# Kernel optimization log

Hardware: AMD Instinct MI355X
Metric: run time of the kernel (lower is better)

Reference implementation:

```python
import jax, jax.numpy as jnp
import numpy as np

HEADS = 8
DIM_HEAD = 64

def setup_inputs() -> dict:
    key = jax.random.key(0)
    ks = jax.random.split(key, 9)
    B, N1, N2, D = 4, 2048, 2048, 1024
    inner = HEADS * DIM_HEAD  # 512
    s_in = 1.0 / np.sqrt(D)
    s_inner = 1.0 / np.sqrt(inner)
    return {
        "x1": jax.random.normal(ks[0], (B, N1, D), jnp.float32),
        "x2": jax.random.normal(ks[1], (B, N2, D), jnp.float32),
        "Wq1": jax.random.normal(ks[2], (D, inner), jnp.float32) * s_in,
        "Wk1": jax.random.normal(ks[3], (D, inner), jnp.float32) * s_in,
        "Wv1": jax.random.normal(ks[4], (D, inner), jnp.float32) * s_in,
        "Wk2": jax.random.normal(ks[5], (D, inner), jnp.float32) * s_in,
        "Wv2": jax.random.normal(ks[6], (D, inner), jnp.float32) * s_in,
        "Wo": jax.random.normal(ks[7], (inner, D), jnp.float32) * s_inner,
        "bo": jnp.zeros((D,), jnp.float32),
    }

def reference(x1, x2, Wq1, Wk1, Wv1, Wk2, Wv2, Wo, bo):
    h, d = HEADS, DIM_HEAD
    scale = d ** (-0.5)
    B, N1, _ = x1.shape
    N2 = x2.shape[1]

    def split_heads(t, n):
        return t.reshape(B, n, h, d)  # [B, n, h, d]

    q1 = split_heads(x1 @ Wq1, N1)
    k1 = split_heads(x1 @ Wk1, N1)
    v1 = split_heads(x1 @ Wv1, N1)
    k2 = split_heads(x2 @ Wk2, N2)
    v2 = split_heads(x2 @ Wv2, N2)

    k = jnp.concatenate([k1, k2], axis=1)  # [B, N1+N2, h, d]
    v = jnp.concatenate([v1, v2], axis=1)

    # fp32 precision for QK^T (matches _ATTN_PRECISION == 'fp32')
    sim = jnp.einsum('bihd,bjhd->bhij', q1.astype(jnp.float32),
                     k.astype(jnp.float32)) * scale  # [B, h, N1, N1+N2]
    attn = jax.nn.softmax(sim, axis=-1)
    out = jnp.einsum('bhij,bjhd->bihd', attn, v)  # [B, N1, h, d]
    out = out.reshape(B, N1, h * d)
    return out @ Wo + bo
```

## Files before the change

### kernel.cpp

```cpp
#include <hip/hip_runtime.h>
#include <stdint.h>

typedef __bf16 bf16x8 __attribute__((ext_vector_type(8)));
typedef float f32x4 __attribute__((ext_vector_type(4)));
typedef unsigned short ushort_t;

#define MFMA16(a,b,c) __builtin_amdgcn_mfma_f32_16x16x32_bf16((a),(b),(c),0,0,0)

__device__ __forceinline__ unsigned short f2bf(float f){
    unsigned u = __builtin_bit_cast(unsigned, f);
    u += 0x7fffu + ((u>>16)&1u);
    return (unsigned short)(u>>16);
}
__device__ __forceinline__ unsigned pack2bf(float lo, float hi){
    unsigned a = __builtin_bit_cast(unsigned, lo) + 0x8000u;
    unsigned b = __builtin_bit_cast(unsigned, hi) + 0x8000u;
    return __builtin_amdgcn_perm(b, a, 0x07060302u);
}
__device__ __forceinline__ float fexp2(float x){
#if __has_builtin(__builtin_amdgcn_exp2f)
    return __builtin_amdgcn_exp2f(x);
#else
    return exp2f(x);
#endif
}

__device__ __forceinline__ void async16(ushort_t* lds, const ushort_t* g){
#if __has_builtin(__builtin_amdgcn_global_load_lds)
    __builtin_amdgcn_global_load_lds(
        (const __attribute__((address_space(1))) void*)g,
        (__attribute__((address_space(3))) void*)lds, 16, 0, 0);
#else
    const int l = (int)(threadIdx.x & 63u);
    *(uint4*)(lds + (size_t)l*8) = *(const uint4*)g;
#endif
}

__global__ __launch_bounds__(256) void convert_x(const float* __restrict__ src,
                                                 ushort_t* __restrict__ dst){
    size_t i = ((size_t)blockIdx.x*256 + threadIdx.x)*8;
    float4 a = *(const float4*)(src + i);
    float4 b = *(const float4*)(src + i + 4);
    uint4 o;
    o.x = pack2bf(a.x, a.y); o.y = pack2bf(a.z, a.w);
    o.z = pack2bf(b.x, b.y); o.w = pack2bf(b.z, b.w);
    *(uint4*)(dst + i) = o;
}

__global__ __launch_bounds__(256) void transpose_w(
    const float* __restrict__ w0, const float* __restrict__ w1,
    const float* __restrict__ w2, const float* __restrict__ w3,
    const float* __restrict__ w4,
    ushort_t* __restrict__ Wt1, ushort_t* __restrict__ Wt2)
{
    int z = blockIdx.z;
    const float* src; ushort_t* dst;
    if (z < 3)  { src = (z==0)?w0:((z==1)?w1:w2); dst = Wt1 + (size_t)z*512*1024; }
    else        { src = (z==3)?w3:w4;             dst = Wt2 + (size_t)(z-3)*512*1024; }
    const int K = 1024, N = 512;
    int k0 = blockIdx.x*32, n0 = blockIdx.y*32;
    __shared__ float T[32][33];
    int t = threadIdx.x;
    int kr = t>>3, nc = (t&7)*4;
    float4 v = *(const float4*)(src + (size_t)(k0+kr)*N + n0 + nc);
    T[kr][nc] = v.x; T[kr][nc+1] = v.y; T[kr][nc+2] = v.z; T[kr][nc+3] = v.w;
    __syncthreads();
    int nr = t>>3, kc = (t&7)*4;
    uint2 o;
    o.x = pack2bf(T[kc][nr],   T[kc+1][nr]);
    o.y = pack2bf(T[kc+2][nr], T[kc+3][nr]);
    *(uint2*)(dst + (size_t)(n0+nr)*K + k0 + kc) = o;
    (void)K;
}

__global__ __launch_bounds__(256) void transpose_wo(
    const float* __restrict__ src, ushort_t* __restrict__ dst)
{
    __shared__ float T[64][33];
    const int k0 = blockIdx.x*64;
    const int n0 = blockIdx.y*32;
    const int t = threadIdx.x;
    const int kr = t>>3, nc = (t&7)*4;
#pragma unroll
    for (int hf = 0; hf < 2; ++hf){
        float4 v = *(const float4*)(src + (size_t)(k0 + hf*32 + kr)*1024 + n0 + nc);
        T[hf*32+kr][nc]   = v.x; T[hf*32+kr][nc+1] = v.y;
        T[hf*32+kr][nc+2] = v.z; T[hf*32+kr][nc+3] = v.w;
    }
    __syncthreads();
    const int nr = t>>3, kc = (t&7)*8;
    ushort_t tmp[8];
#pragma unroll
    for (int e = 0; e < 8; ++e){
        int dp = kc + e;
        int d  = ((dp&3)<<4) | (dp>>2);
        tmp[e] = f2bf(T[d][nr]);
    }
    *(uint4*)(dst + (size_t)(n0+nr)*512 + k0 + kc) = *(uint4*)tmp;
}

template<int KD, int MODE>
__global__ __launch_bounds__(256) void gemm_bt(
    const ushort_t* __restrict__ A, const ushort_t* __restrict__ Bt,
    ushort_t* __restrict__ Qp, ushort_t* __restrict__ Kp, ushort_t* __restrict__ Vtp,
    float* __restrict__ outF, const float* __restrict__ bias, int koff)
{
    __shared__ ushort_t As[2][128][32];
    __shared__ ushort_t Bs[2][128][32];
    const int t = threadIdx.x;
    const int m0 = blockIdx.x*128, n0 = blockIdx.y*128;
    const int w = t>>6, l = t&63;
    const int quad = l>>4, lc = l&15;
    const int wr = (w>>1)*64, wc = (w&1)*64;

    f32x4 acc[4][4] = {};

    const int crow = l>>2;
    const int kseg = (l&3)*8;
    const ushort_t* gA0 = A  + (size_t)(m0 + w*32      + crow)*KD + kseg;
    const ushort_t* gA1 = A  + (size_t)(m0 + w*32 + 16 + crow)*KD + kseg;
    const ushort_t* gB0 = Bt + (size_t)(n0 + w*32      + crow)*KD + kseg;
    const ushort_t* gB1 = Bt + (size_t)(n0 + w*32 + 16 + crow)*KD + kseg;

    const int NK = KD/32;

    async16(&As[0][w*32][0],    gA0);
    async16(&As[0][w*32+16][0], gA1);
    async16(&Bs[0][w*32][0],    gB0);
    async16(&Bs[0][w*32+16][0], gB1);
    __syncthreads();

    for (int kk = 0; kk < NK; ++kk) {
        const int cur = kk & 1;
        if (kk + 1 < NK) {
            const int k0 = (kk+1)*32;
            const int nx = cur ^ 1;
            async16(&As[nx][w*32][0],    gA0 + k0);
            async16(&As[nx][w*32+16][0], gA1 + k0);
            async16(&Bs[nx][w*32][0],    gB0 + k0);
            async16(&Bs[nx][w*32+16][0], gB1 + k0);
        }
        bf16x8 af[4], bfv[4];
#pragma unroll
        for (int i = 0; i < 4; ++i) {
            af[i]  = *(const bf16x8*)&As[cur][wr + i*16 + lc][quad*8];
            bfv[i] = *(const bf16x8*)&Bs[cur][wc + i*16 + lc][quad*8];
        }
#pragma unroll
        for (int mt = 0; mt < 4; ++mt)
#pragma unroll
            for (int nt = 0; nt < 4; ++nt)
                acc[mt][nt] = MFMA16(af[mt], bfv[nt], acc[mt][nt]);
        __syncthreads();
    }

    if (MODE == 2) {
        float bv[4];
#pragma unroll
        for (int nt = 0; nt < 4; ++nt) bv[nt] = bias[n0 + wc + nt*16 + lc];
#pragma unroll
        for (int mt = 0; mt < 4; ++mt) {
            const int row = m0 + wr + mt*16 + quad*4;
#pragma unroll
            for (int nt = 0; nt < 4; ++nt) {
                const int col = n0 + wc + nt*16 + lc;
#pragma unroll
                for (int r = 0; r < 4; ++r)
                    outF[(size_t)(row+r)*1024 + col] = acc[mt][nt][r] + bv[nt];
            }
        }
    } else {
        const int sub = (MODE == 0) ? (n0>>9) : (1 + (n0>>9));
        const int hh  = ((n0 + wc)>>6) & 7;
        const int dp  = 4*lc;
        const float QSC = 0.18033688011112042f;
        if (sub == 0) {
#pragma unroll
            for (int mt = 0; mt < 4; ++mt) {
                const int row = m0 + wr + mt*16 + quad*4;
                const int b = row>>11, i = row & 2047;
#pragma unroll
                for (int r = 0; r < 4; ++r) {
                    uint2 o;
                    o.x = pack2bf(acc[mt][0][r]*QSC, acc[mt][1][r]*QSC);
                    o.y = pack2bf(acc[mt][2][r]*QSC, acc[mt][3][r]*QSC);
                    *(uint2*)(Qp + ((size_t)(b*8+hh)*2048 + i + r)*64 + dp) = o;
                }
            }
        } else if (sub == 1) {
#pragma unroll
            for (int mt = 0; mt < 4; ++mt) {
                const int row = m0 + wr + mt*16 + quad*4;
                const int b = row>>11, i = row & 2047;
#pragma unroll
                for (int r = 0; r < 4; ++r) {
                    uint2 o;
                    o.x = pack2bf(acc[mt][0][r], acc[mt][1][r]);
                    o.y = pack2bf(acc[mt][2][r], acc[mt][3][r]);
                    *(uint2*)(Kp + ((size_t)(b*8+hh)*4096 + koff + i + r)*64 + dp) = o;
                }
            }
        } else {
#pragma unroll
            for (int mt = 0; mt < 4; ++mt) {
                const int row = m0 + wr + mt*16 + quad*4;
                const int b = row>>11, i = row & 2047;
#pragma unroll
                for (int nt = 0; nt < 4; ++nt) {
                    uint2 o;
                    o.x = pack2bf(acc[mt][nt][0], acc[mt][nt][1]);
                    o.y = pack2bf(acc[mt][nt][2], acc[mt][nt][3]);
                    *(uint2*)(Vtp + ((size_t)(b*8+hh)*64 + dp + nt)*4096 + koff + i) = o;
                }
            }
        }
    }
}

template<int SPLIT>
__global__ __launch_bounds__(256) void flash_attn_k(
    const ushort_t* __restrict__ Q, const ushort_t* __restrict__ Kg,
    const ushort_t* __restrict__ Vt, ushort_t* __restrict__ AO,
    float* __restrict__ P0, float* __restrict__ P1, float* __restrict__ Lp)
{
    constexpr int NJT = 64 / SPLIT;
    __shared__ ushort_t Ks[2][64][72];
    __shared__ ushort_t Vs[2][64][72];
    const int bh = blockIdx.x, qt = blockIdx.y;
    const int sp = (SPLIT > 1) ? (int)blockIdx.z : 0;
    const int jt0 = sp * NJT;
    const int b = bh>>3, h = bh&7;
    const int t = threadIdx.x, wv = t>>6, l = t&63;
    const int quad = l>>4, lc = l&15;

    const ushort_t* qbase = Q + ((size_t)bh*2048 + qt*128 + wv*16 + lc)*64;
    bf16x8 qA0 = *(const bf16x8*)(qbase + quad*8);
    bf16x8 qA1 = *(const bf16x8*)(qbase + 32 + quad*8);
    bf16x8 qB0 = *(const bf16x8*)(qbase + 64*64 + quad*8);
    bf16x8 qB1 = *(const bf16x8*)(qbase + 64*64 + 32 + quad*8);

    const ushort_t* Kb = Kg + (size_t)bh*4096*64;
    const ushort_t* Vb = Vt + (size_t)bh*64*4096;

    const int srow   = t>>2;
    const int schunk = t&3;
    const ushort_t* kst = Kb + (size_t)srow*64   + schunk*16;
    const ushort_t* vst = Vb + (size_t)srow*4096 + schunk*16;
    const int vcol = (schunk>>1)*32 + (schunk&1)*4;

    float l0 = 0.0f, l1 = 0.0f;
    f32x4 o0[4] = {}, o1[4] = {};

    const size_t kq0 = (size_t)jt0*64;
    uint4 ka  = *(const uint4*)(kst + kq0*64);
    uint4 kb2 = *(const uint4*)(kst + kq0*64 + 8);
    uint4 va  = *(const uint4*)(vst + kq0);
    uint4 vb2 = *(const uint4*)(vst + kq0 + 8);

    for (int jt = 0; jt < NJT; ++jt) {
        const int cur = jt & 1;
        ushort_t* ksd = &Ks[cur][srow][schunk*16];
        ushort_t* vsd = &Vs[cur][srow][vcol];
        *(uint4*)ksd     = ka;
        *(uint4*)(ksd+8) = kb2;
        { uint2 t0; t0.x = va.x;  t0.y = va.y;  *(uint2*)(vsd)      = t0; }
        { uint2 t1; t1.x = va.z;  t1.y = va.w;  *(uint2*)(vsd + 8)  = t1; }
        { uint2 t2; t2.x = vb2.x; t2.y = vb2.y; *(uint2*)(vsd + 16) = t2; }
        { uint2 t3; t3.x = vb2.z; t3.y = vb2.w; *(uint2*)(vsd + 24) = t3; }
        __syncthreads();
        if (jt < NJT - 1) {
            const size_t j0 = (size_t)(jt0 + jt + 1)*64;
            ka  = *(const uint4*)(kst + j0*64);
            kb2 = *(const uint4*)(kst + j0*64 + 8);
            va  = *(const uint4*)(vst + j0);
            vb2 = *(const uint4*)(vst + j0 + 8);
        }

        f32x4 s0[4], s1[4];
#pragma unroll
        for (int kt = 0; kt < 4; ++kt) {
            bf16x8 kf0 = *(const bf16x8*)&Ks[cur][kt*16 + lc][quad*8];
            bf16x8 kf1 = *(const bf16x8*)&Ks[cur][kt*16 + lc][32 + quad*8];
            f32x4 z0 = {}, z1 = {};
            z0 = MFMA16(kf0, qA0, z0); z0 = MFMA16(kf1, qA1, z0);
            z1 = MFMA16(kf0, qB0, z1); z1 = MFMA16(kf1, qB1, z1);
            s0[kt] = z0; s1[kt] = z1;
        }

        union { unsigned u[8]; bf16x8 v[2]; } p0, p1;
        float rs0 = 0.0f, rs1 = 0.0f;
#pragma unroll
        for (int kt = 0; kt < 4; ++kt) {
            float a0 = fexp2(s0[kt][0]), a1v = fexp2(s0[kt][1]);
            float a2 = fexp2(s0[kt][2]), a3 = fexp2(s0[kt][3]);
            rs0 += (a0 + a1v) + (a2 + a3);
            p0.u[kt*2]   = pack2bf(a0, a1v);
            p0.u[kt*2+1] = pack2bf(a2, a3);
            float c0 = fexp2(s1[kt][0]), c1 = fexp2(s1[kt][1]);
            float c2 = fexp2(s1[kt][2]), c3 = fexp2(s1[kt][3]);
            rs1 += (c0 + c1) + (c2 + c3);
            p1.u[kt*2]   = pack2bf(c0, c1);
            p1.u[kt*2+1] = pack2bf(c2, c3);
        }
        l0 += rs0; l1 += rs1;

#pragma unroll
        for (int dt = 0; dt < 4; ++dt) {
            bf16x8 vf0 = *(const bf16x8*)&Vs[cur][dt*16 + lc][quad*8];
            bf16x8 vf1 = *(const bf16x8*)&Vs[cur][dt*16 + lc][32 + quad*8];
            o0[dt] = MFMA16(vf0, p0.v[0], o0[dt]);
            o0[dt] = MFMA16(vf1, p0.v[1], o0[dt]);
            o1[dt] = MFMA16(vf0, p1.v[0], o1[dt]);
            o1[dt] = MFMA16(vf1, p1.v[1], o1[dt]);
        }
    }

    l0 += __shfl_xor(l0, 16); l0 += __shfl_xor(l0, 32);
    l1 += __shfl_xor(l1, 16); l1 += __shfl_xor(l1, 32);

    if (SPLIT == 1) {
        float li0 = 1.0f / l0, li1 = 1.0f / l1;
        const int qA = qt*128 + wv*16 + lc;
        ushort_t* aodA = AO + ((size_t)b*2048 + qA)*512 + h*64 + quad*4;
        ushort_t* aodB = aodA + (size_t)64*512;
#pragma unroll
        for (int dt = 0; dt < 4; ++dt) {
            uint2 oa, ob;
            oa.x = pack2bf(o0[dt][0]*li0, o0[dt][1]*li0);
            oa.y = pack2bf(o0[dt][2]*li0, o0[dt][3]*li0);
            *(uint2*)(aodA + dt*16) = oa;
            ob.x = pack2bf(o1[dt][0]*li1, o1[dt][1]*li1);
            ob.y = pack2bf(o1[dt][2]*li1, o1[dt][3]*li1);
            *(uint2*)(aodB + dt*16) = ob;
        }
    } else {
        float* P = sp ? P1 : P0;
        const int bid = bh*16 + qt;
        const int qrA = wv*16 + lc;
        const size_t pbA = ((size_t)bid*128 + qrA)*64;
        const size_t pbB = pbA + (size_t)64*64;
#pragma unroll
        for (int dt = 0; dt < 4; ++dt) {
            *(f32x4*)(P + pbA + dt*16 + quad*4) = o0[dt];
            *(f32x4*)(P + pbB + dt*16 + quad*4) = o1[dt];
        }
        if (l < 16) {
            Lp[((size_t)sp*512 + bid)*128 + qrA]      = l0;
            Lp[((size_t)sp*512 + bid)*128 + 64 + qrA] = l1;
        }
    }
}

__global__ __launch_bounds__(256) void combine_attn(
    const float* __restrict__ P0, const float* __restrict__ P1,
    const float* __restrict__ Lp, ushort_t* __restrict__ AO)
{
    const int bid = blockIdx.x;
    const int bh = bid>>4, qt = bid&15;
    const int b = bh>>3, h = bh&7;
    const int t = threadIdx.x;
    const int dcol = (t&15)*4;
    const size_t pblk = (size_t)bid*8192;
#pragma unroll
    for (int e = 0; e < 8; ++e) {
        const int qrow = e*16 + (t>>4);
        const size_t idx = pblk + (size_t)qrow*64 + dcol;
        float4 a = *(const float4*)(P0 + idx);
        float4 c = *(const float4*)(P1 + idx);
        float ls = Lp[(size_t)bid*128 + qrow] + Lp[(size_t)(512 + bid)*128 + qrow];
        float inv = 1.0f / ls;
        uint2 o;
        o.x = pack2bf((a.x + c.x)*inv, (a.y + c.y)*inv);
        o.y = pack2bf((a.z + c.z)*inv, (a.w + c.w)*inv);
        ushort_t* ao = AO + ((size_t)b*2048 + qt*128 + qrow)*512 + h*64 + dcol;
        *(uint2*)ao = o;
    }
}

extern "C" void kernel_launch(void* const* d_in, const int* in_sizes, int n_in,
                              void* d_out, int out_size, void* d_ws, size_t ws_size,
                              hipStream_t stream)
{
    const float* x1  = (const float*)d_in[0];
    const float* x2  = (const float*)d_in[1];
    const float* Wq1 = (const float*)d_in[2];
    const float* Wk1 = (const float*)d_in[3];
    const float* Wv1 = (const float*)d_in[4];
    const float* Wk2 = (const float*)d_in[5];
    const float* Wv2 = (const float*)d_in[6];
    const float* Wo  = (const float*)d_in[7];
    const float* bo  = (const float*)d_in[8];
    float* out = (float*)d_out;

    ushort_t* ws  = (ushort_t*)d_ws;
    ushort_t* Xc1 = ws;
    ushort_t* Xc2 = Xc1 + 8388608;
    ushort_t* Wt1 = Xc2 + 8388608;
    ushort_t* Wt2 = Wt1 + 1572864;
    ushort_t* Wot = Wt2 + 1048576;
    ushort_t* Qp  = Wot + 524288;
    ushort_t* Kp  = Qp  + 4194304;
    ushort_t* Vtp = Kp  + 8388608;
    ushort_t* Pex = Vtp + 8388608;
    ushort_t* Lex = Pex + 8388608;
    ushort_t* AOp = Xc2;

    convert_x<<<4096, 256, 0, stream>>>(x1, Xc1);
    convert_x<<<4096, 256, 0, stream>>>(x2, Xc2);
    transpose_w<<<dim3(32,16,5), 256, 0, stream>>>(Wq1,Wk1,Wv1,Wk2,Wv2, Wt1,Wt2);
    transpose_wo<<<dim3(8,32), 256, 0, stream>>>(Wo, Wot);

    gemm_bt<1024,0><<<dim3(64,12), 256, 0, stream>>>(Xc1, Wt1, Qp, Kp, Vtp, nullptr, nullptr, 0);
    gemm_bt<1024,1><<<dim3(64,8),  256, 0, stream>>>(Xc2, Wt2, Qp, Kp, Vtp, nullptr, nullptr, 2048);

    const size_t NEED = 99090432ull;
    if (ws_size >= NEED) {
        float* P0f = (float*)Xc1;
        float* P1f = (float*)Pex;
        float* Lf  = (float*)Lex;
        flash_attn_k<2><<<dim3(32,16,2), 256, 0, stream>>>(Qp, Kp, Vtp, nullptr, P0f, P1f, Lf);
        combine_attn<<<512, 256, 0, stream>>>(P0f, P1f, Lf, AOp);
    } else {
        flash_attn_k<1><<<dim3(32,16,1), 256, 0, stream>>>(Qp, Kp, Vtp, AOp, nullptr, nullptr, nullptr);
    }

    gemm_bt<512,2><<<dim3(64,8), 256, 0, stream>>>(AOp, Wot, nullptr, nullptr, nullptr, out, bo, 0);
}
```

Baseline: 307.2 us.

## Use async direct-to-LDS K/V loads with XOR-swizzled shared tiles

Replaces the register-staged K/V prefetch with async 16-byte global-to-LDS copies into double buffers, with one barrier per iteration. The padded shared arrays become unpadded tiles addressed with an XOR swizzle. The V projection epilogue writes a permuted row order so the swizzled reads still form correct MFMA fragments. It also fuses exp2 into the QK loop and requests 4 blocks per CU through launch bounds, aiming to cut register pressure and copy instructions. The risks are a wrong permutation producing bad results, and register spills from the tighter bound.

```diff
diff --git a/kernel.cpp b/kernel.cpp
--- a/kernel.cpp
+++ b/kernel.cpp
@@ -205,12 +205,13 @@
             for (int mt = 0; mt < 4; ++mt) {
                 const int row = m0 + wr + mt*16 + quad*4;
                 const int b = row>>11, i = row & 2047;
+                const int ip = (i & ~28) | (((i>>2)&3)<<3) | (((i>>4)&1)<<2);
 #pragma unroll
                 for (int nt = 0; nt < 4; ++nt) {
                     uint2 o;
                     o.x = pack2bf(acc[mt][nt][0], acc[mt][nt][1]);
                     o.y = pack2bf(acc[mt][nt][2], acc[mt][nt][3]);
-                    *(uint2*)(Vtp + ((size_t)(b*8+hh)*64 + dp + nt)*4096 + koff + i) = o;
+                    *(uint2*)(Vtp + ((size_t)(b*8+hh)*64 + dp + nt)*4096 + koff + ip) = o;
                 }
             }
         }
@@ -218,14 +219,14 @@
 }
 
 template<int SPLIT>
-__global__ __launch_bounds__(256) void flash_attn_k(
+__global__ __launch_bounds__(256, 4) void flash_attn_k(
     const ushort_t* __restrict__ Q, const ushort_t* __restrict__ Kg,
     const ushort_t* __restrict__ Vt, ushort_t* __restrict__ AO,
     float* __restrict__ P0, float* __restrict__ P1, float* __restrict__ Lp)
 {
     constexpr int NJT = 64 / SPLIT;
-    __shared__ ushort_t Ks[2][64][72];
-    __shared__ ushort_t Vs[2][64][72];
+    __shared__ ushort_t Ks[2][64][64];
+    __shared__ ushort_t Vs[2][64][64];
     const int bh = blockIdx.x, qt = blockIdx.y;
     const int sp = (SPLIT > 1) ? (int)blockIdx.z : 0;
     const int jt0 = sp * NJT;
@@ -242,62 +243,56 @@
     const ushort_t* Kb = Kg + (size_t)bh*4096*64;
     const ushort_t* Vb = Vt + (size_t)bh*64*4096;
 
-    const int srow   = t>>2;
-    const int schunk = t&3;
-    const ushort_t* kst = Kb + (size_t)srow*64   + schunk*16;
-    const ushort_t* vst = Vb + (size_t)srow*4096 + schunk*16;
-    const int vcol = (schunk>>1)*32 + (schunk&1)*4;
+    const int r8 = l>>3;
+    const int sc = (l&7) ^ r8;
+    const ushort_t* kg0 = Kb + ((size_t)jt0*64 + wv*16 + r8)*64 + sc*8;
+    const ushort_t* kg1 = kg0 + (size_t)8*64;
+    const ushort_t* vg0 = Vb + (size_t)(wv*16 + r8)*4096 + (size_t)jt0*64 + sc*8;
+    const ushort_t* vg1 = vg0 + (size_t)8*4096;
+
+    const int swA = ((quad       ^ (lc&7)) << 3);
+    const int swB = (((quad ^ 4) ^ (lc&7)) << 3);
 
     float l0 = 0.0f, l1 = 0.0f;
     f32x4 o0[4] = {}, o1[4] = {};
 
-    const size_t kq0 = (size_t)jt0*64;
-    uint4 ka  = *(const uint4*)(kst + kq0*64);
-    uint4 kb2 = *(const uint4*)(kst + kq0*64 + 8);
-    uint4 va  = *(const uint4*)(vst + kq0);
-    uint4 vb2 = *(const uint4*)(vst + kq0 + 8);
+    async16(&Ks[0][wv*16][0],   kg0);
+    async16(&Ks[0][wv*16+8][0], kg1);
+    async16(&Vs[0][wv*16][0],   vg0);
+    async16(&Vs[0][wv*16+8][0], vg1);
+    __syncthreads();
 
     for (int jt = 0; jt < NJT; ++jt) {
         const int cur = jt & 1;
-        ushort_t* ksd = &Ks[cur][srow][schunk*16];
-        ushort_t* vsd = &Vs[cur][srow][vcol];
-        *(uint4*)ksd     = ka;
-        *(uint4*)(ksd+8) = kb2;
-        { uint2 t0; t0.x = va.x;  t0.y = va.y;  *(uint2*)(vsd)      = t0; }
-        { uint2 t1; t1.x = va.z;  t1.y = va.w;  *(uint2*)(vsd + 8)  = t1; }
-        { uint2 t2; t2.x = vb2.x; t2.y = vb2.y; *(uint2*)(vsd + 16) = t2; }
-        { uint2 t3; t3.x = vb2.z; t3.y = vb2.w; *(uint2*)(vsd + 24) = t3; }
-        __syncthreads();
-        if (jt < NJT - 1) {
-            const size_t j0 = (size_t)(jt0 + jt + 1)*64;
-            ka  = *(const uint4*)(kst + j0*64);
-            kb2 = *(const uint4*)(kst + j0*64 + 8);
-            va  = *(const uint4*)(vst + j0);
-            vb2 = *(const uint4*)(vst + j0 + 8);
-        }
-
-        f32x4 s0[4], s1[4];
+        if (jt + 1 < NJT) {
+            const int nx = cur ^ 1;
+            const size_t ko = (size_t)(jt+1)*4096;
+            const size_t vo = (size_t)(jt+1)*64;
+            async16(&Ks[nx][wv*16][0],   kg0 + ko);
+            async16(&Ks[nx][wv*16+8][0], kg1 + ko);
+            async16(&Vs[nx][wv*16][0],   vg0 + vo);
+            async16(&Vs[nx][wv*16+8][0], vg1 + vo);
+        }
+        const ushort_t* KsC = &Ks[cur][0][0];
+        const ushort_t* VsC = &Vs[cur][0][0];
+
+        union { unsigned u[8]; bf16x8 v[2]; } p0, p1;
+        float rs0 = 0.0f, rs1 = 0.0f;
 #pragma unroll
         for (int kt = 0; kt < 4; ++kt) {
-            bf16x8 kf0 = *(const bf16x8*)&Ks[cur][kt*16 + lc][quad*8];
-            bf16x8 kf1 = *(const bf16x8*)&Ks[cur][kt*16 + lc][32 + quad*8];
+            const int ro = (kt*16 + lc)*64;
+            bf16x8 kf0 = *(const bf16x8*)(KsC + ro + swA);
+            bf16x8 kf1 = *(const bf16x8*)(KsC + ro + swB);
             f32x4 z0 = {}, z1 = {};
             z0 = MFMA16(kf0, qA0, z0); z0 = MFMA16(kf1, qA1, z0);
             z1 = MFMA16(kf0, qB0, z1); z1 = MFMA16(kf1, qB1, z1);
-            s0[kt] = z0; s1[kt] = z1;
-        }
-
-        union { unsigned u[8]; bf16x8 v[2]; } p0, p1;
-        float rs0 = 0.0f, rs1 = 0.0f;
-#pragma unroll
-        for (int kt = 0; kt < 4; ++kt) {
-            float a0 = fexp2(s0[kt][0]), a1v = fexp2(s0[kt][1]);
-            float a2 = fexp2(s0[kt][2]), a3 = fexp2(s0[kt][3]);
+            float a0 = fexp2(z0[0]), a1v = fexp2(z0[1]);
+            float a2 = fexp2(z0[2]), a3 = fexp2(z0[3]);
             rs0 += (a0 + a1v) + (a2 + a3);
             p0.u[kt*2]   = pack2bf(a0, a1v);
             p0.u[kt*2+1] = pack2bf(a2, a3);
-            float c0 = fexp2(s1[kt][0]), c1 = fexp2(s1[kt][1]);
-            float c2 = fexp2(s1[kt][2]), c3 = fexp2(s1[kt][3]);
+            float c0 = fexp2(z1[0]), c1 = fexp2(z1[1]);
+            float c2 = fexp2(z1[2]), c3 = fexp2(z1[3]);
             rs1 += (c0 + c1) + (c2 + c3);
             p1.u[kt*2]   = pack2bf(c0, c1);
             p1.u[kt*2+1] = pack2bf(c2, c3);
@@ -306,13 +301,15 @@
 
 #pragma unroll
         for (int dt = 0; dt < 4; ++dt) {
-            bf16x8 vf0 = *(const bf16x8*)&Vs[cur][dt*16 + lc][quad*8];
-            bf16x8 vf1 = *(const bf16x8*)&Vs[cur][dt*16 + lc][32 + quad*8];
+            const int ro = (dt*16 + lc)*64;
+            bf16x8 vf0 = *(const bf16x8*)(VsC + ro + swA);
+            bf16x8 vf1 = *(const bf16x8*)(VsC + ro + swB);
             o0[dt] = MFMA16(vf0, p0.v[0], o0[dt]);
             o0[dt] = MFMA16(vf1, p0.v[1], o0[dt]);
             o1[dt] = MFMA16(vf0, p1.v[0], o1[dt]);
             o1[dt] = MFMA16(vf1, p1.v[1], o1[dt]);
         }
+        __syncthreads();
     }
 
     l0 += __shfl_xor(l0, 16); l0 += __shfl_xor(l0, 32);
```

Measured after the change: 295.1 us. -4.0%, faster.
